# Optimization experiments

Hardware: AMD Instinct MI355X
Metric: run time of the kernel (lower is better)

The kernel has to match this reference:

```python
import jax, jax.numpy as jnp
import numpy as np

N, T, D, H = 32, 2048, 256, 256


def setup_inputs() -> dict:
    key = jax.random.key(0)
    k0, k1, k2, k3, k4 = jax.random.split(key, 5)
    std = 1.0 / np.sqrt(H + D)  # matches PTLSTM.reset()
    return {
        "x": jax.random.normal(k0, (N, T, D), dtype=jnp.float32),
        "state": jnp.zeros((N, 2 * H), dtype=jnp.float32),  # [h0 | c0]
        "w_ih": (jax.random.normal(k1, (4 * H, D)) * std).astype(jnp.float32),
        "w_hh": (jax.random.normal(k2, (4 * H, H)) * std).astype(jnp.float32),
        "b_ih": (jax.random.normal(k3, (4 * H,)) * std).astype(jnp.float32),
        "b_hh": (jax.random.normal(k4, (4 * H,)) * std).astype(jnp.float32),
    }


def reference(x, state, w_ih, w_hh, b_ih, b_hh):
    # Single-layer batch_first LSTM, PyTorch gate order (i, f, g, o).
    Hd = w_hh.shape[1]
    h0, c0 = state[:, :Hd], state[:, Hd:]
    # Precompute input-to-hidden projection for all timesteps (one big GEMM).
    xg = jnp.einsum('ntd,gd->ntg', x, w_ih) + (b_ih + b_hh)  # [N, T, 4H]

    def step(carry, xg_t):
        h, c = carry
        gates = xg_t + h @ w_hh.T  # [N, 4H]
        i, f, g, o = jnp.split(gates, 4, axis=-1)
        i = jax.nn.sigmoid(i)
        f = jax.nn.sigmoid(f)
        g = jnp.tanh(g)
        o = jax.nn.sigmoid(o)
        c = f * c + i * g
        h = o * jnp.tanh(c)
        return (h, c), h

    (hT, cT), out_t = jax.lax.scan(step, (h0, c0), jnp.swapaxes(xg, 0, 1))
    output = jnp.swapaxes(out_t, 0, 1)  # [N, T, H]
    outstate = jnp.concatenate([hT, cT], axis=1)  # [N, 2H]
    return output, outstate
```

## Files before the change

kernel.cpp:

```cpp
#include <hip/hip_runtime.h>

typedef _Float16 half2_t __attribute__((ext_vector_type(2)));
typedef __bf16   bf16x8  __attribute__((ext_vector_type(8)));
typedef float    f32x4   __attribute__((ext_vector_type(4)));
typedef unsigned short u16x8 __attribute__((ext_vector_type(8)));
typedef unsigned int  uint32;
typedef unsigned long long uint64;

#define LSTM_N 32
#define LSTM_T 2048
#define LSTM_D 256
#define LSTM_H 256
#define NG 1024
#define CH 256
#define NCH (LSTM_T / CH)
#define MCH (LSTM_N * CH)

#define OFF_XG   ((size_t)0)
#define SZ_XG    ((size_t)MCH * NG * 4)
#define OFF_WIHB (OFF_XG + SZ_XG)
#define SZ_WIHB  ((size_t)NG * LSTM_D * 2)
#define OFF_BIAS (OFF_WIHB + SZ_WIHB)
#define SZ_BIAS  ((size_t)4096)
#define OFF_WPK  (OFF_BIAS + SZ_BIAS)
#define SZ_WPK   ((size_t)2 * 32 * 512 * 16)
#define OFF_CST  (OFF_WPK + SZ_WPK)
#define SZ_CST   ((size_t)LSTM_N * 256 * 4)
#define OFF_HST  (OFF_CST + SZ_CST)
#define SZ_HST   ((size_t)LSTM_N * 128 * 4)
#define OFF_HX   (OFF_HST + SZ_HST)
#define SZ_HX    ((size_t)LSTM_N * 2 * 2 * 64 * 8)

#if defined(__has_builtin)
#if __has_builtin(__builtin_amdgcn_fdot2)
#define HAVE_FDOT2 1
#endif
#endif

__device__ __forceinline__ float fdot2(uint32 w, uint32 h, float acc) {
#ifdef HAVE_FDOT2
  return __builtin_amdgcn_fdot2(__builtin_bit_cast(half2_t, w),
                                __builtin_bit_cast(half2_t, h), acc, false);
#else
  half2_t wv = __builtin_bit_cast(half2_t, w);
  half2_t hv = __builtin_bit_cast(half2_t, h);
  float r = fmaf((float)wv.x, (float)hv.x, acc);
  return fmaf((float)wv.y, (float)hv.y, r);
#endif
}

__device__ __forceinline__ float sigm(float x) { return 1.f / (1.f + __expf(-x)); }
__device__ __forceinline__ float tanh_fast(float x) { return 2.f / (1.f + __expf(-2.f * x)) - 1.f; }

__device__ __forceinline__ unsigned short f2bf(float f) {
  uint32 u = __builtin_bit_cast(uint32, f);
  uint32 r = (u + 0x7FFFu + ((u >> 16) & 1u)) >> 16;
  return (unsigned short)r;
}

__device__ __forceinline__ float bfly8(const float a[8], int kap) {
  float k0[4], g0[4];
  const bool b4 = (kap & 4) != 0;
#pragma unroll
  for (int v = 0; v < 4; ++v) {
    k0[v] = b4 ? a[v + 4] : a[v];
    g0[v] = b4 ? a[v] : a[v + 4];
  }
#pragma unroll
  for (int v = 0; v < 4; ++v) k0[v] += __shfl_xor(g0[v], 4, 64);
  float k1[2], g1[2];
  const bool b2 = (kap & 2) != 0;
#pragma unroll
  for (int v = 0; v < 2; ++v) {
    k1[v] = b2 ? k0[v + 2] : k0[v];
    g1[v] = b2 ? k0[v] : k0[v + 2];
  }
#pragma unroll
  for (int v = 0; v < 2; ++v) k1[v] += __shfl_xor(g1[v], 2, 64);
  const bool b1 = (kap & 1) != 0;
  float k2 = b1 ? k1[1] : k1[0];
  float g2 = b1 ? k1[0] : k1[1];
  return k2 + __shfl_xor(g2, 1, 64);
}


__global__ void cvt_bf16_k(const float* __restrict__ src, unsigned short* __restrict__ dst, int n) {
  int i = blockIdx.x * blockDim.x + threadIdx.x;
  if (4 * i + 3 < n) {
    float4 v = ((const float4*)src)[i];
    ushort4 o;
    o.x = f2bf(v.x); o.y = f2bf(v.y); o.z = f2bf(v.z); o.w = f2bf(v.w);
    ((ushort4*)dst)[i] = o;
  }
}

__global__ void bias_sum_k(const float* __restrict__ bih, const float* __restrict__ bhh,
                           float* __restrict__ bias) {
  int g = blockIdx.x * blockDim.x + threadIdx.x;
  if (g < NG) bias[g] = bih[g] + bhh[g];
}

__global__ void wpack_k(const float* __restrict__ whh, uint32* __restrict__ wpk) {
  int e = blockIdx.x * blockDim.x + threadIdx.x;
  int p = e >> 16;
  int rem = e & 0xFFFF;
  int i = rem >> 9;
  int t = rem & 511;
  int rho = i >> 4, j = i & 15;
  int kap = t & 7, rg = t >> 3;
  int lr = 8 * rg + rho;
  int q = lr >> 7, u = lr & 127;
  int r = q * 256 + 128 * p + u;
  int k = (j < 8) ? (128 * p + 16 * kap + 2 * j)
                  : (128 * (1 - p) + 16 * kap + 2 * (j - 8));
  half2_t h;
  h.x = (_Float16)whh[r * 256 + k];
  h.y = (_Float16)whh[r * 256 + k + 1];
  wpk[((p * 32 + (i >> 2)) * 512 + t) * 4 + (i & 3)] = __builtin_bit_cast(uint32, h);
}

__global__ void state_init_k(const float* __restrict__ state, float* __restrict__ cst,
                             uint32* __restrict__ hst, uint64* __restrict__ hx) {
  int i = blockIdx.x * blockDim.x + threadIdx.x;
  int n = i >> 8, j = i & 255;
  cst[i] = state[n * 512 + 256 + j];
  if ((j & 1) == 0) {
    half2_t h2;
    h2.x = (_Float16)state[n * 512 + j];
    h2.y = (_Float16)state[n * 512 + j + 1];
    hst[(n << 7) + (j >> 1)] = __builtin_bit_cast(uint32, h2);
  }
  hx[i] = 0ull;
}

__global__ __launch_bounds__(256) void gemm_xg(const float* __restrict__ x,
                                               const unsigned short* __restrict__ wb,
                                               const float* __restrict__ bias,
                                               float* __restrict__ xg, int ch) {
  __shared__ unsigned short As[128 * 40];
  __shared__ unsigned short Bs[128 * 40];
  const int tid = threadIdx.x;
  const int m0 = blockIdx.y * 128;
  const int g0 = blockIdx.x * 128;
  const int w = tid >> 6;
  const int lane = tid & 63;
  const int wm = (w >> 1) * 64, wn = (w & 1) * 64;
  const int row_l = tid >> 2;
  const int q = tid & 3;
  const int lr = lane & 15, kg = lane >> 4;

  size_t grow[2];
#pragma unroll
  for (int r = 0; r < 2; ++r) {
    int gm = m0 + row_l + 64 * r;
    grow[r] = (size_t)(gm >> 8) * LSTM_T + (size_t)ch * CH + (gm & 255);
  }

  f32x4 acc[4][4];
#pragma unroll
  for (int i = 0; i < 4; ++i)
#pragma unroll
    for (int j = 0; j < 4; ++j) acc[i][j] = (f32x4){0.f, 0.f, 0.f, 0.f};

  for (int kt = 0; kt < 8; ++kt) {
#pragma unroll
    for (int r = 0; r < 2; ++r) {
      int row = row_l + 64 * r;
      const float* ap = x + grow[r] * 256 + kt * 32 + q * 8;
      float4 v0 = *(const float4*)ap;
      float4 v1 = *(const float4*)(ap + 4);
      u16x8 o;
      o[0] = f2bf(v0.x); o[1] = f2bf(v0.y); o[2] = f2bf(v0.z); o[3] = f2bf(v0.w);
      o[4] = f2bf(v1.x); o[5] = f2bf(v1.y); o[6] = f2bf(v1.z); o[7] = f2bf(v1.w);
      *(uint4*)((char*)As + row * 80 + q * 16) = __builtin_bit_cast(uint4, o);
      uint4 bv = *(const uint4*)(wb + (size_t)(g0 + row) * 256 + kt * 32 + q * 8);
      *(uint4*)((char*)Bs + row * 80 + q * 16) = bv;
    }
    __syncthreads();
    bf16x8 af[4], bfr[4];
#pragma unroll
    for (int i = 0; i < 4; ++i)
      af[i] = __builtin_bit_cast(bf16x8, *(const uint4*)((char*)As + (wm + 16 * i + lr) * 80 + kg * 16));
#pragma unroll
    for (int j = 0; j < 4; ++j)
      bfr[j] = __builtin_bit_cast(bf16x8, *(const uint4*)((char*)Bs + (wn + 16 * j + lr) * 80 + kg * 16));
#pragma unroll
    for (int i = 0; i < 4; ++i)
#pragma unroll
      for (int j = 0; j < 4; ++j)
        acc[i][j] = __builtin_amdgcn_mfma_f32_16x16x32_bf16(af[i], bfr[j], acc[i][j], 0, 0, 0);
    __syncthreads();
  }
#pragma unroll
  for (int j = 0; j < 4; ++j) {
    int gc = g0 + wn + 16 * j + lr;
    float bj = bias[gc];
#pragma unroll
    for (int i = 0; i < 4; ++i) {
#pragma unroll
      for (int r = 0; r < 4; ++r) {
        int m = m0 + wm + 16 * i + kg * 4 + r;
        xg[(size_t)m * NG + gc] = acc[i][j][r] + bj;
      }
    }
  }
}

__global__ __launch_bounds__(512, 2) void lstm_scan(const float* __restrict__ xg,
                                                    const uint4* __restrict__ wpk4,
                                                    float* __restrict__ cst,
                                                    uint32* __restrict__ hst,
                                                    uint64* __restrict__ hx,
                                                    float* __restrict__ out, int ch) {
  __shared__ float actb[512];
  __shared__ uint32 hbuf[128];

  const int tid = threadIdx.x;
  const int b = blockIdx.x;
  const int n = b & 31;
  const int p = b >> 5;
  const int kap = tid & 7;
  const int rg = tid >> 3;
  const int lrf = 8 * rg + kap;
  const int q = lrf >> 7, u = lrf & 127;
  const int grow = q * 256 + 128 * p + u;

  uint32 wr[128];
#pragma unroll
  for (int ig = 0; ig < 32; ++ig) {
    uint4 v = wpk4[(p * 32 + ig) * 512 + tid];
    wr[4 * ig + 0] = v.x; wr[4 * ig + 1] = v.y; wr[4 * ig + 2] = v.z; wr[4 * ig + 3] = v.w;
  }
  float c = 0.f;
  if (tid < 128) {
    c = cst[n * 256 + 128 * p + tid];
    hbuf[tid] = hst[n * 128 + tid];
  }
  __syncthreads();

  const float* xgn = xg + (size_t)n * CH * NG;
  float* outb = out + ((size_t)n * LSTM_T + (size_t)ch * CH) * LSTM_H;
  uint64* hx_own  = hx + (size_t)((n * 2 + p) * 2) * 64;
  uint64* hx_peer = hx + (size_t)((n * 2 + (1 - p)) * 2) * 64;
  const int gsbase = ch * CH;
  const int ownbase  = 64 * p + 8 * kap;
  const int peerbase = 64 * (1 - p) + 8 * kap;

  float xpre = xgn[grow];

  for (int tt = 0; tt < CH; ++tt) {
    if (tt > 0 && tid < 64) {
      const uint32 gs = (uint32)(gsbase + tt);
      uint64 v;
      do {
        v = __hip_atomic_load(&hx_peer[(gs & 1) * 64 + tid], __ATOMIC_RELAXED,
                              __HIP_MEMORY_SCOPE_AGENT);
      } while ((uint32)(v >> 32) != gs);
      hbuf[64 * (1 - p) + tid] = (uint32)v;
    }
    uint32 hro[8];
    *(uint4*)&hro[0] = *(const uint4*)&hbuf[ownbase];
    *(uint4*)&hro[4] = *(const uint4*)&hbuf[ownbase + 4];
    float acc[8];
#pragma unroll
    for (int rho = 0; rho < 8; ++rho) {
      float a = 0.f;
#pragma unroll
      for (int j = 0; j < 8; ++j) a = fdot2(wr[rho * 16 + j], hro[j], a);
      acc[rho] = a;
    }
    __syncthreads();
    uint32 hrp[8];
    *(uint4*)&hrp[0] = *(const uint4*)&hbuf[peerbase];
    *(uint4*)&hrp[4] = *(const uint4*)&hbuf[peerbase + 4];
#pragma unroll
    for (int rho = 0; rho < 8; ++rho) {
      float a = acc[rho];
#pragma unroll
      for (int j = 0; j < 8; ++j) a = fdot2(wr[rho * 16 + 8 + j], hrp[j], a);
      acc[rho] = a;
    }
    float s = bfly8(acc, kap);
    float pre = s + xpre;
    if (tt < CH - 1) xpre = xgn[(size_t)(tt + 1) * NG + grow];
    float a0 = (q == 2) ? tanh_fast(pre) : sigm(pre);
    actb[lrf] = a0;
    __syncthreads();
    if (tid < 128) {
      float gi = actb[tid];
      float gf = actb[128 + tid];
      float gg = actb[256 + tid];
      float go = actb[384 + tid];
      c = gf * c + gi * gg;
      float h = go * tanh_fast(c);
      _Float16 hf = (_Float16)h;
      ((unsigned short*)hbuf)[128 * p + tid] = __builtin_bit_cast(unsigned short, hf);
      outb[(size_t)tt * LSTM_H + 128 * p + tid] = h;
      if (ch == NCH - 1 && tt == CH - 1) {
        float* os = out + (size_t)LSTM_N * LSTM_T * LSTM_H + n * 512;
        os[128 * p + tid] = h;
        os[256 + 128 * p + tid] = c;
      }
    }
    __syncthreads();
    if (tt < CH - 1 && tid < 64) {
      const uint32 gs = (uint32)(gsbase + tt + 1);
      uint64 v = (uint64)hbuf[64 * p + tid] | ((uint64)gs << 32);
      __hip_atomic_store(&hx_own[(gs & 1) * 64 + tid], v, __ATOMIC_RELAXED,
                         __HIP_MEMORY_SCOPE_AGENT);
    }
  }
  if (tid < 128) cst[n * 256 + 128 * p + tid] = c;
  if (tid < 64) hst[n * 128 + 64 * p + tid] = hbuf[64 * p + tid];
}

extern "C" void kernel_launch(void* const* d_in, const int* in_sizes, int n_in,
                              void* d_out, int out_size, void* d_ws, size_t ws_size,
                              hipStream_t stream) {
  const float* x   = (const float*)d_in[0];
  const float* st  = (const float*)d_in[1];
  const float* wih = (const float*)d_in[2];
  const float* whh = (const float*)d_in[3];
  const float* bih = (const float*)d_in[4];
  const float* bhh = (const float*)d_in[5];
  float* out = (float*)d_out;
  char* ws = (char*)d_ws;

  float* xg = (float*)(ws + OFF_XG);
  unsigned short* wihb = (unsigned short*)(ws + OFF_WIHB);
  float* bias = (float*)(ws + OFF_BIAS);
  uint32* wpk = (uint32*)(ws + OFF_WPK);
  float* cst = (float*)(ws + OFF_CST);
  uint32* hst = (uint32*)(ws + OFF_HST);
  uint64* hx = (uint64*)(ws + OFF_HX);

  cvt_bf16_k<<<(NG * LSTM_D / 4 + 255) / 256, 256, 0, stream>>>(wih, wihb, NG * LSTM_D);
  bias_sum_k<<<4, 256, 0, stream>>>(bih, bhh, bias);
  wpack_k<<<512, 256, 0, stream>>>(whh, wpk);
  state_init_k<<<32, 256, 0, stream>>>(st, cst, hst, hx);

  for (int ch = 0; ch < NCH; ++ch) {
    gemm_xg<<<dim3(NG / 128, MCH / 128), 256, 0, stream>>>(x, wihb, bias, xg, ch);
    lstm_scan<<<64, 512, 0, stream>>>(xg, (const uint4*)wpk, cst, hst, hx, out, ch);
  }
}
```

Before: 3.450 ms.

## Run recurrent matvec on MFMA with 16-sequence batches per block

The recurrent h@W_hh product now uses f16 MFMA instructions. Each block handles 16 batch sequences and one half of the hidden units, instead of one sequence per block using fdot2 and butterfly shuffles. The xg GEMM output is transposed to a gate-major layout so each lane can load its gate preactivations directly. Gate activations and the cell update are done in registers, which removes the shared-memory activation exchange and one barrier per step. Only 4 of the 16 launched blocks do work, so far fewer CUs run the serial scan, and the peer exchange per step now moves more data through atomics.

```diff
diff --git a/kernel.cpp b/kernel.cpp
--- a/kernel.cpp
+++ b/kernel.cpp
@@ -1,6 +1,7 @@
 #include <hip/hip_runtime.h>
 
 typedef _Float16 half2_t __attribute__((ext_vector_type(2)));
+typedef _Float16 f16x8   __attribute__((ext_vector_type(8)));
 typedef __bf16   bf16x8  __attribute__((ext_vector_type(8)));
 typedef float    f32x4   __attribute__((ext_vector_type(4)));
 typedef unsigned short u16x8 __attribute__((ext_vector_type(8)));
@@ -17,7 +18,7 @@
 #define MCH (LSTM_N * CH)
 
 #define OFF_XG   ((size_t)0)
-#define SZ_XG    ((size_t)MCH * NG * 4)
+#define SZ_XG    ((size_t)NG * MCH * 4)
 #define OFF_WIHB (OFF_XG + SZ_XG)
 #define SZ_WIHB  ((size_t)NG * LSTM_D * 2)
 #define OFF_BIAS (OFF_WIHB + SZ_WIHB)
@@ -29,25 +30,7 @@
 #define OFF_HST  (OFF_CST + SZ_CST)
 #define SZ_HST   ((size_t)LSTM_N * 128 * 4)
 #define OFF_HX   (OFF_HST + SZ_HST)
-#define SZ_HX    ((size_t)LSTM_N * 2 * 2 * 64 * 8)
-
-#if defined(__has_builtin)
-#if __has_builtin(__builtin_amdgcn_fdot2)
-#define HAVE_FDOT2 1
-#endif
-#endif
-
-__device__ __forceinline__ float fdot2(uint32 w, uint32 h, float acc) {
-#ifdef HAVE_FDOT2
-  return __builtin_amdgcn_fdot2(__builtin_bit_cast(half2_t, w),
-                                __builtin_bit_cast(half2_t, h), acc, false);
-#else
-  half2_t wv = __builtin_bit_cast(half2_t, w);
-  half2_t hv = __builtin_bit_cast(half2_t, h);
-  float r = fmaf((float)wv.x, (float)hv.x, acc);
-  return fmaf((float)wv.y, (float)hv.y, r);
-#endif
-}
+#define SZ_HX    ((size_t)2 * 2 * 2 * 1024 * 8)
 
 __device__ __forceinline__ float sigm(float x) { return 1.f / (1.f + __expf(-x)); }
 __device__ __forceinline__ float tanh_fast(float x) { return 2.f / (1.f + __expf(-2.f * x)) - 1.f; }
@@ -56,31 +39,6 @@
   uint32 u = __builtin_bit_cast(uint32, f);
   uint32 r = (u + 0x7FFFu + ((u >> 16) & 1u)) >> 16;
   return (unsigned short)r;
-}
-
-__device__ __forceinline__ float bfly8(const float a[8], int kap) {
-  float k0[4], g0[4];
-  const bool b4 = (kap & 4) != 0;
-#pragma unroll
-  for (int v = 0; v < 4; ++v) {
-    k0[v] = b4 ? a[v + 4] : a[v];
-    g0[v] = b4 ? a[v] : a[v + 4];
-  }
-#pragma unroll
-  for (int v = 0; v < 4; ++v) k0[v] += __shfl_xor(g0[v], 4, 64);
-  float k1[2], g1[2];
-  const bool b2 = (kap & 2) != 0;
-#pragma unroll
-  for (int v = 0; v < 2; ++v) {
-    k1[v] = b2 ? k0[v + 2] : k0[v];
-    g1[v] = b2 ? k0[v] : k0[v + 2];
-  }
-#pragma unroll
-  for (int v = 0; v < 2; ++v) k1[v] += __shfl_xor(g1[v], 2, 64);
-  const bool b1 = (kap & 1) != 0;
-  float k2 = b1 ? k1[1] : k1[0];
-  float g2 = b1 ? k1[0] : k1[1];
-  return k2 + __shfl_xor(g2, 1, 64);
 }
 
 
@@ -103,20 +61,17 @@
 __global__ void wpack_k(const float* __restrict__ whh, uint32* __restrict__ wpk) {
   int e = blockIdx.x * blockDim.x + threadIdx.x;
   int p = e >> 16;
-  int rem = e & 0xFFFF;
-  int i = rem >> 9;
-  int t = rem & 511;
-  int rho = i >> 4, j = i & 15;
-  int kap = t & 7, rg = t >> 3;
-  int lr = 8 * rg + rho;
-  int q = lr >> 7, u = lr & 127;
-  int r = q * 256 + 128 * p + u;
-  int k = (j < 8) ? (128 * p + 16 * kap + 2 * j)
-                  : (128 * (1 - p) + 16 * kap + 2 * (j - 8));
+  int i = (e >> 9) & 127;
+  int t = e & 511;
+  int q = i >> 5, kc = (i >> 2) & 7, rr = i & 3;
+  int w = t >> 6, l = t & 63;
+  int grow = q * 256 + 128 * p + 16 * w + (l & 15);
+  int kb = (kc < 4) ? (128 * p + 32 * kc) : (128 * (1 - p) + 32 * (kc - 4));
+  int k = kb + (l >> 4) * 8 + 2 * rr;
   half2_t h;
-  h.x = (_Float16)whh[r * 256 + k];
-  h.y = (_Float16)whh[r * 256 + k + 1];
-  wpk[((p * 32 + (i >> 2)) * 512 + t) * 4 + (i & 3)] = __builtin_bit_cast(uint32, h);
+  h.x = (_Float16)whh[grow * 256 + k];
+  h.y = (_Float16)whh[grow * 256 + k + 1];
+  wpk[((p * 32 + q * 8 + kc) * 512 + t) * 4 + rr] = __builtin_bit_cast(uint32, h);
 }
 
 __global__ void state_init_k(const float* __restrict__ state, float* __restrict__ cst,
@@ -133,28 +88,25 @@
   hx[i] = 0ull;
 }
 
-__global__ __launch_bounds__(256) void gemm_xg(const float* __restrict__ x,
-                                               const unsigned short* __restrict__ wb,
-                                               const float* __restrict__ bias,
-                                               float* __restrict__ xg, int ch) {
+__global__ __launch_bounds__(256) void gemm_xgp(const float* __restrict__ x,
+                                                const unsigned short* __restrict__ wb,
+                                                const float* __restrict__ bias,
+                                                float* __restrict__ xgp, int ch) {
   __shared__ unsigned short As[128 * 40];
   __shared__ unsigned short Bs[128 * 40];
   const int tid = threadIdx.x;
   const int m0 = blockIdx.y * 128;
-  const int g0 = blockIdx.x * 128;
+  const int c0 = blockIdx.x * 128;
   const int w = tid >> 6;
   const int lane = tid & 63;
   const int wm = (w >> 1) * 64, wn = (w & 1) * 64;
-  const int row_l = tid >> 2;
-  const int q = tid & 3;
   const int lr = lane & 15, kg = lane >> 4;
-
-  size_t grow[2];
-#pragma unroll
-  for (int r = 0; r < 2; ++r) {
-    int gm = m0 + row_l + 64 * r;
-    grow[r] = (size_t)(gm >> 8) * LSTM_T + (size_t)ch * CH + (gm & 255);
-  }
+  const int srow = tid >> 1, kh = tid & 1;
+
+  const int cbl = c0 + srow;
+  const float* xb = x + (size_t)(cbl & 31) * LSTM_T * LSTM_D
+                      + (size_t)(ch * CH + (cbl >> 5)) * LSTM_D + kh * 16;
+  const unsigned short* ab = wb + (size_t)(m0 + srow) * 256 + kh * 16;
 
   f32x4 acc[4][4];
 #pragma unroll
@@ -163,18 +115,23 @@
     for (int j = 0; j < 4; ++j) acc[i][j] = (f32x4){0.f, 0.f, 0.f, 0.f};
 
   for (int kt = 0; kt < 8; ++kt) {
-#pragma unroll
-    for (int r = 0; r < 2; ++r) {
-      int row = row_l + 64 * r;
-      const float* ap = x + grow[r] * 256 + kt * 32 + q * 8;
-      float4 v0 = *(const float4*)ap;
-      float4 v1 = *(const float4*)(ap + 4);
-      u16x8 o;
-      o[0] = f2bf(v0.x); o[1] = f2bf(v0.y); o[2] = f2bf(v0.z); o[3] = f2bf(v0.w);
-      o[4] = f2bf(v1.x); o[5] = f2bf(v1.y); o[6] = f2bf(v1.z); o[7] = f2bf(v1.w);
-      *(uint4*)((char*)As + row * 80 + q * 16) = __builtin_bit_cast(uint4, o);
-      uint4 bv = *(const uint4*)(wb + (size_t)(g0 + row) * 256 + kt * 32 + q * 8);
-      *(uint4*)((char*)Bs + row * 80 + q * 16) = bv;
+    {
+      uint4 a0 = *(const uint4*)(ab + kt * 32);
+      uint4 a1 = *(const uint4*)(ab + kt * 32 + 8);
+      *(uint4*)((char*)As + srow * 80 + kh * 32) = a0;
+      *(uint4*)((char*)As + srow * 80 + kh * 32 + 16) = a1;
+      const float* bp = xb + kt * 32;
+      float4 v0 = *(const float4*)(bp + 0);
+      float4 v1 = *(const float4*)(bp + 4);
+      float4 v2 = *(const float4*)(bp + 8);
+      float4 v3 = *(const float4*)(bp + 12);
+      u16x8 o0, o1;
+      o0[0] = f2bf(v0.x); o0[1] = f2bf(v0.y); o0[2] = f2bf(v0.z); o0[3] = f2bf(v0.w);
+      o0[4] = f2bf(v1.x); o0[5] = f2bf(v1.y); o0[6] = f2bf(v1.z); o0[7] = f2bf(v1.w);
+      o1[0] = f2bf(v2.x); o1[1] = f2bf(v2.y); o1[2] = f2bf(v2.z); o1[3] = f2bf(v2.w);
+      o1[4] = f2bf(v3.x); o1[5] = f2bf(v3.y); o1[6] = f2bf(v3.z); o1[7] = f2bf(v3.w);
+      *(uint4*)((char*)Bs + srow * 80 + kh * 32) = __builtin_bit_cast(uint4, o0);
+      *(uint4*)((char*)Bs + srow * 80 + kh * 32 + 16) = __builtin_bit_cast(uint4, o1);
     }
     __syncthreads();
     bf16x8 af[4], bfr[4];
@@ -191,127 +148,154 @@
         acc[i][j] = __builtin_amdgcn_mfma_f32_16x16x32_bf16(af[i], bfr[j], acc[i][j], 0, 0, 0);
     __syncthreads();
   }
-#pragma unroll
-  for (int j = 0; j < 4; ++j) {
-    int gc = g0 + wn + 16 * j + lr;
-    float bj = bias[gc];
-#pragma unroll
-    for (int i = 0; i < 4; ++i) {
-#pragma unroll
-      for (int r = 0; r < 4; ++r) {
-        int m = m0 + wm + 16 * i + kg * 4 + r;
-        xg[(size_t)m * NG + gc] = acc[i][j][r] + bj;
-      }
-    }
-  }
-}
-
-__global__ __launch_bounds__(512, 2) void lstm_scan(const float* __restrict__ xg,
+  float bias_v[4][4];
+#pragma unroll
+  for (int i = 0; i < 4; ++i)
+#pragma unroll
+    for (int r = 0; r < 4; ++r) bias_v[i][r] = bias[m0 + wm + 16 * i + kg * 4 + r];
+#pragma unroll
+  for (int i = 0; i < 4; ++i)
+#pragma unroll
+    for (int j = 0; j < 4; ++j)
+#pragma unroll
+      for (int r = 0; r < 4; ++r)
+        xgp[(size_t)(m0 + wm + 16 * i + kg * 4 + r) * MCH + (c0 + wn + 16 * j + lr)]
+            = acc[i][j][r] + bias_v[i][r];
+}
+
+__global__ __launch_bounds__(512, 2) void lstm_scan(const float* __restrict__ xgp,
                                                     const uint4* __restrict__ wpk4,
                                                     float* __restrict__ cst,
                                                     uint32* __restrict__ hst,
                                                     uint64* __restrict__ hx,
                                                     float* __restrict__ out, int ch) {
-  __shared__ float actb[512];
-  __shared__ uint32 hbuf[128];
-
-  const int tid = threadIdx.x;
+  __shared__ uint32 hbuf[16][132];
   const int b = blockIdx.x;
-  const int n = b & 31;
-  const int p = b >> 5;
-  const int kap = tid & 7;
-  const int rg = tid >> 3;
-  const int lrf = 8 * rg + kap;
-  const int q = lrf >> 7, u = lrf & 127;
-  const int grow = q * 256 + 128 * p + u;
-
-  uint32 wr[128];
-#pragma unroll
-  for (int ig = 0; ig < 32; ++ig) {
-    uint4 v = wpk4[(p * 32 + ig) * 512 + tid];
-    wr[4 * ig + 0] = v.x; wr[4 * ig + 1] = v.y; wr[4 * ig + 2] = v.z; wr[4 * ig + 3] = v.w;
-  }
-  float c = 0.f;
-  if (tid < 128) {
-    c = cst[n * 256 + 128 * p + tid];
-    hbuf[tid] = hst[n * 128 + tid];
-  }
+  if ((b & 7) >= 2) return;
+  const int g = b & 1;
+  const int p = b >> 3;
+  const int t = threadIdx.x;
+  const int w = t >> 6, l = t & 63;
+  const int ls = l & 15, lq = l >> 4;
+
+  uint4 wfr[32];
+#pragma unroll
+  for (int i = 0; i < 32; ++i) wfr[i] = wpk4[(p * 32 + i) * 512 + t];
+
+  {
+    int s = t >> 5, m4 = (t & 31) * 4;
+    *(uint4*)&hbuf[s][m4] = *(const uint4*)&hst[(16 * g + s) * 128 + m4];
+  }
+  const int ubase = 16 * w + 4 * lq;
+  const int n = 16 * g + ls;
+  float4 cc4 = *(const float4*)&cst[n * 256 + 128 * p + ubase];
+  float cc[4] = {cc4.x, cc4.y, cc4.z, cc4.w};
   __syncthreads();
 
-  const float* xgn = xg + (size_t)n * CH * NG;
-  float* outb = out + ((size_t)n * LSTM_T + (size_t)ch * CH) * LSTM_H;
-  uint64* hx_own  = hx + (size_t)((n * 2 + p) * 2) * 64;
-  uint64* hx_peer = hx + (size_t)((n * 2 + (1 - p)) * 2) * 64;
   const int gsbase = ch * CH;
-  const int ownbase  = 64 * p + 8 * kap;
-  const int peerbase = 64 * (1 - p) + 8 * kap;
-
-  float xpre = xgn[grow];
+  uint64* hx_own  = hx + (size_t)(g * 2 + p) * 2048;
+  uint64* hx_peer = hx + (size_t)(g * 2 + (1 - p)) * 2048;
+
+  const int rowb = 128 * p + ubase;
+  const float* xgl = xgp + (size_t)rowb * MCH + n;
+  float* outb = out + ((size_t)n * LSTM_T + (size_t)ch * CH) * 256 + 128 * p + ubase;
+
+  const int own_u32 = 64 * p;
+  const int peer_u32 = 64 * (1 - p);
+  const int slotb = ls * 64 + 8 * w + 2 * lq;
+
+  float xpre[16];
+#pragma unroll
+  for (int q = 0; q < 4; ++q)
+#pragma unroll
+    for (int r = 0; r < 4; ++r)
+      xpre[q * 4 + r] = xgl[(size_t)(q * 256 + r) * MCH];
 
   for (int tt = 0; tt < CH; ++tt) {
-    if (tt > 0 && tid < 64) {
+    f32x4 acc[4];
+#pragma unroll
+    for (int q = 0; q < 4; ++q) acc[q] = (f32x4){0.f, 0.f, 0.f, 0.f};
+    uint4 bb[4];
+#pragma unroll
+    for (int kc = 0; kc < 4; ++kc)
+      bb[kc] = *(const uint4*)&hbuf[ls][own_u32 + 16 * kc + 4 * lq];
+#pragma unroll
+    for (int kc = 0; kc < 4; ++kc) {
+      f16x8 bv = __builtin_bit_cast(f16x8, bb[kc]);
+#pragma unroll
+      for (int q = 0; q < 4; ++q)
+        acc[q] = __builtin_amdgcn_mfma_f32_16x16x32_f16(
+            __builtin_bit_cast(f16x8, wfr[q * 8 + kc]), bv, acc[q], 0, 0, 0);
+    }
+    if (tt > 0) {
       const uint32 gs = (uint32)(gsbase + tt);
-      uint64 v;
+      uint64* sp = &hx_peer[(size_t)(gs & 1) * 1024 + 2 * t];
+      uint64 v0, v1;
       do {
-        v = __hip_atomic_load(&hx_peer[(gs & 1) * 64 + tid], __ATOMIC_RELAXED,
-                              __HIP_MEMORY_SCOPE_AGENT);
-      } while ((uint32)(v >> 32) != gs);
-      hbuf[64 * (1 - p) + tid] = (uint32)v;
-    }
-    uint32 hro[8];
-    *(uint4*)&hro[0] = *(const uint4*)&hbuf[ownbase];
-    *(uint4*)&hro[4] = *(const uint4*)&hbuf[ownbase + 4];
-    float acc[8];
-#pragma unroll
-    for (int rho = 0; rho < 8; ++rho) {
-      float a = 0.f;
-#pragma unroll
-      for (int j = 0; j < 8; ++j) a = fdot2(wr[rho * 16 + j], hro[j], a);
-      acc[rho] = a;
+        v0 = __hip_atomic_load(sp, __ATOMIC_RELAXED, __HIP_MEMORY_SCOPE_AGENT);
+      } while ((uint32)(v0 >> 32) != gs);
+      do {
+        v1 = __hip_atomic_load(sp + 1, __ATOMIC_RELAXED, __HIP_MEMORY_SCOPE_AGENT);
+      } while ((uint32)(v1 >> 32) != gs);
+      uint2 pv; pv.x = (uint32)v0; pv.y = (uint32)v1;
+      *(uint2*)&hbuf[t >> 5][peer_u32 + 2 * (t & 31)] = pv;
     }
     __syncthreads();
-    uint32 hrp[8];
-    *(uint4*)&hrp[0] = *(const uint4*)&hbuf[peerbase];
-    *(uint4*)&hrp[4] = *(const uint4*)&hbuf[peerbase + 4];
-#pragma unroll
-    for (int rho = 0; rho < 8; ++rho) {
-      float a = acc[rho];
-#pragma unroll
-      for (int j = 0; j < 8; ++j) a = fdot2(wr[rho * 16 + 8 + j], hrp[j], a);
-      acc[rho] = a;
-    }
-    float s = bfly8(acc, kap);
-    float pre = s + xpre;
-    if (tt < CH - 1) xpre = xgn[(size_t)(tt + 1) * NG + grow];
-    float a0 = (q == 2) ? tanh_fast(pre) : sigm(pre);
-    actb[lrf] = a0;
+#pragma unroll
+    for (int kc = 0; kc < 4; ++kc)
+      bb[kc] = *(const uint4*)&hbuf[ls][peer_u32 + 16 * kc + 4 * lq];
+#pragma unroll
+    for (int kc = 0; kc < 4; ++kc) {
+      f16x8 bv = __builtin_bit_cast(f16x8, bb[kc]);
+#pragma unroll
+      for (int q = 0; q < 4; ++q)
+        acc[q] = __builtin_amdgcn_mfma_f32_16x16x32_f16(
+            __builtin_bit_cast(f16x8, wfr[q * 8 + 4 + kc]), bv, acc[q], 0, 0, 0);
+    }
+    float hv[4];
+#pragma unroll
+    for (int r = 0; r < 4; ++r) {
+      float gi = sigm(acc[0][r] + xpre[0 + r]);
+      float gf = sigm(acc[1][r] + xpre[4 + r]);
+      float gg = tanh_fast(acc[2][r] + xpre[8 + r]);
+      float go = sigm(acc[3][r] + xpre[12 + r]);
+      float c2 = gf * cc[r] + gi * gg;
+      cc[r] = c2;
+      hv[r] = go * tanh_fast(c2);
+    }
+    half2_t h01, h23;
+    h01.x = (_Float16)hv[0]; h01.y = (_Float16)hv[1];
+    h23.x = (_Float16)hv[2]; h23.y = (_Float16)hv[3];
+    uint32 hu0 = __builtin_bit_cast(uint32, h01);
+    uint32 hu1 = __builtin_bit_cast(uint32, h23);
+    if (tt < CH - 1) {
+      const uint32 gs2 = (uint32)(gsbase + tt + 1);
+      uint64* dp = &hx_own[(size_t)(gs2 & 1) * 1024 + slotb];
+      __hip_atomic_store(dp, (uint64)hu0 | ((uint64)gs2 << 32),
+                         __ATOMIC_RELAXED, __HIP_MEMORY_SCOPE_AGENT);
+      __hip_atomic_store(dp + 1, (uint64)hu1 | ((uint64)gs2 << 32),
+                         __ATOMIC_RELAXED, __HIP_MEMORY_SCOPE_AGENT);
+    }
+    uint2 hw; hw.x = hu0; hw.y = hu1;
+    *(uint2*)&hbuf[ls][own_u32 + 8 * w + 2 * lq] = hw;
+    *(float4*)&outb[(size_t)tt * 256] = make_float4(hv[0], hv[1], hv[2], hv[3]);
+    if (ch == NCH - 1 && tt == CH - 1) {
+      float* os = out + (size_t)LSTM_N * LSTM_T * LSTM_H + n * 512 + 128 * p + ubase;
+      *(float4*)os = make_float4(hv[0], hv[1], hv[2], hv[3]);
+      *(float4*)(os + 256) = make_float4(cc[0], cc[1], cc[2], cc[3]);
+    }
+    if (tt < CH - 1) {
+#pragma unroll
+      for (int q = 0; q < 4; ++q)
+#pragma unroll
+        for (int r = 0; r < 4; ++r)
+          xpre[q * 4 + r] = xgl[(size_t)(q * 256 + r) * MCH + (size_t)(tt + 1) * 32];
+    }
     __syncthreads();
-    if (tid < 128) {
-      float gi = actb[tid];
-      float gf = actb[128 + tid];
-      float gg = actb[256 + tid];
-      float go = actb[384 + tid];
-      c = gf * c + gi * gg;
-      float h = go * tanh_fast(c);
-      _Float16 hf = (_Float16)h;
-      ((unsigned short*)hbuf)[128 * p + tid] = __builtin_bit_cast(unsigned short, hf);
-      outb[(size_t)tt * LSTM_H + 128 * p + tid] = h;
-      if (ch == NCH - 1 && tt == CH - 1) {
-        float* os = out + (size_t)LSTM_N * LSTM_T * LSTM_H + n * 512;
-        os[128 * p + tid] = h;
-        os[256 + 128 * p + tid] = c;
-      }
-    }
-    __syncthreads();
-    if (tt < CH - 1 && tid < 64) {
-      const uint32 gs = (uint32)(gsbase + tt + 1);
-      uint64 v = (uint64)hbuf[64 * p + tid] | ((uint64)gs << 32);
-      __hip_atomic_store(&hx_own[(gs & 1) * 64 + tid], v, __ATOMIC_RELAXED,
-                         __HIP_MEMORY_SCOPE_AGENT);
-    }
-  }
-  if (tid < 128) cst[n * 256 + 128 * p + tid] = c;
-  if (tid < 64) hst[n * 128 + 64 * p + tid] = hbuf[64 * p + tid];
+  }
+  *(float4*)&cst[n * 256 + 128 * p + ubase] = make_float4(cc[0], cc[1], cc[2], cc[3]);
+  uint2 hfin = *(uint2*)&hbuf[ls][own_u32 + 8 * w + 2 * lq];
+  *(uint2*)&hst[n * 128 + 64 * p + 8 * w + 2 * lq] = hfin;
 }
 
 extern "C" void kernel_launch(void* const* d_in, const int* in_sizes, int n_in,
@@ -326,7 +310,7 @@
   float* out = (float*)d_out;
   char* ws = (char*)d_ws;
 
-  float* xg = (float*)(ws + OFF_XG);
+  float* xgp = (float*)(ws + OFF_XG);
   unsigned short* wihb = (unsigned short*)(ws + OFF_WIHB);
   float* bias = (float*)(ws + OFF_BIAS);
   uint32* wpk = (uint32*)(ws + OFF_WPK);
@@ -340,7 +324,7 @@
   state_init_k<<<32, 256, 0, stream>>>(st, cst, hst, hx);
 
   for (int ch = 0; ch < NCH; ++ch) {
-    gemm_xg<<<dim3(NG / 128, MCH / 128), 256, 0, stream>>>(x, wihb, bias, xg, ch);
-    lstm_scan<<<64, 512, 0, stream>>>(xg, (const uint4*)wpk, cst, hst, hx, out, ch);
-  }
-}
+    gemm_xgp<<<dim3(MCH / 128, NG / 128), 256, 0, stream>>>(x, wihb, bias, xgp, ch);
+    lstm_scan<<<16, 512, 0, stream>>>(xgp, (const uint4*)wpk, cst, hst, hx, out, ch);
+  }
+}
```

Result: slower. 5.882 ms (+70.5%).

## Have every thread poll peer hidden state directly and double-buffer own h

Applied to the files above, without the earlier changes.

Each thread now loads its eight peer h words straight from the global exchange buffer with atomics and spins on the step tags itself. The own-half dot products run while those loads are in flight. One LDS barrier per step is removed, and the own hidden state moves to a double-buffered shared array. Producer threads pack two fp16 values through a shuffle and publish right after computing h, not after the barrier. The change trades more global polling traffic, since all 512 threads poll instead of 64, for a shorter critical path between the two cooperating blocks. The row mapping also changes, and launch bounds drop to one block per SM.

```diff
diff --git a/kernel.cpp b/kernel.cpp
--- a/kernel.cpp
+++ b/kernel.cpp
@@ -206,112 +206,126 @@
   }
 }
 
-__global__ __launch_bounds__(512, 2) void lstm_scan(const float* __restrict__ xg,
+__global__ __launch_bounds__(512, 1) void lstm_scan(const float* __restrict__ xg,
                                                     const uint4* __restrict__ wpk4,
                                                     float* __restrict__ cst,
                                                     uint32* __restrict__ hst,
                                                     uint64* __restrict__ hx,
                                                     float* __restrict__ out, int ch) {
   __shared__ float actb[512];
-  __shared__ uint32 hbuf[128];
-
-  const int tid = threadIdx.x;
+  __shared__ uint32 hown[2][64];
+
   const int b = blockIdx.x;
   const int n = b & 31;
   const int p = b >> 5;
-  const int kap = tid & 7;
-  const int rg = tid >> 3;
-  const int lrf = 8 * rg + kap;
-  const int q = lrf >> 7, u = lrf & 127;
-  const int grow = q * 256 + 128 * p + u;
+  const int t = threadIdx.x;
+  const int kap = t & 7;
+  const int q = t >> 7;
+  const int u = t & 127;
+  const int R = q * 256 + 128 * p + u;
 
   uint32 wr[128];
 #pragma unroll
   for (int ig = 0; ig < 32; ++ig) {
-    uint4 v = wpk4[(p * 32 + ig) * 512 + tid];
+    uint4 v = wpk4[(p * 32 + ig) * 512 + t];
     wr[4 * ig + 0] = v.x; wr[4 * ig + 1] = v.y; wr[4 * ig + 2] = v.z; wr[4 * ig + 3] = v.w;
   }
   float c = 0.f;
-  if (tid < 128) {
-    c = cst[n * 256 + 128 * p + tid];
-    hbuf[tid] = hst[n * 128 + tid];
-  }
+  if (t < 128) c = cst[n * 256 + 128 * p + t];
+  if (t < 64) hown[0][t] = hst[n * 128 + 64 * p + t];
   __syncthreads();
 
   const float* xgn = xg + (size_t)n * CH * NG;
   float* outb = out + ((size_t)n * LSTM_T + (size_t)ch * CH) * LSTM_H;
-  uint64* hx_own  = hx + (size_t)((n * 2 + p) * 2) * 64;
-  uint64* hx_peer = hx + (size_t)((n * 2 + (1 - p)) * 2) * 64;
+  uint64* hx_own  = hx + (size_t)(n * 2 + p) * 128;
+  uint64* hx_peer = hx + (size_t)(n * 2 + (1 - p)) * 128;
   const int gsbase = ch * CH;
-  const int ownbase  = 64 * p + 8 * kap;
-  const int peerbase = 64 * (1 - p) + 8 * kap;
-
-  float xpre = xgn[grow];
+
+  float xcur = xgn[R];
 
   for (int tt = 0; tt < CH; ++tt) {
-    if (tt > 0 && tid < 64) {
-      const uint32 gs = (uint32)(gsbase + tt);
-      uint64 v;
+    const uint32 gs = (uint32)(gsbase + tt);
+    uint64 pv[8];
+    uint32 hrp[8];
+    if (tt == 0) {
+#pragma unroll
+      for (int m = 0; m < 8; ++m) hrp[m] = hst[n * 128 + 64 * (1 - p) + 8 * kap + m];
+    } else {
+      uint64* sp = &hx_peer[(size_t)(gs & 1) * 64 + 8 * kap];
+#pragma unroll
+      for (int ss = 0; ss < 8; ++ss)
+        pv[ss] = __hip_atomic_load(&sp[ss], __ATOMIC_RELAXED, __HIP_MEMORY_SCOPE_AGENT);
+    }
+    float xnext = (tt < CH - 1) ? xgn[(size_t)(tt + 1) * NG + R] : 0.f;
+    uint32 hro[8];
+    *(uint4*)&hro[0] = *(const uint4*)&hown[tt & 1][8 * kap];
+    *(uint4*)&hro[4] = *(const uint4*)&hown[tt & 1][8 * kap + 4];
+    float acc[8];
+#pragma unroll
+    for (int j = 0; j < 8; ++j) {
+      float a = 0.f;
+#pragma unroll
+      for (int m = 0; m < 8; ++m) a = fdot2(wr[j * 16 + m], hro[m], a);
+      acc[j] = a;
+    }
+    if (tt > 0) {
+      bool ok;
       do {
-        v = __hip_atomic_load(&hx_peer[(gs & 1) * 64 + tid], __ATOMIC_RELAXED,
-                              __HIP_MEMORY_SCOPE_AGENT);
-      } while ((uint32)(v >> 32) != gs);
-      hbuf[64 * (1 - p) + tid] = (uint32)v;
-    }
-    uint32 hro[8];
-    *(uint4*)&hro[0] = *(const uint4*)&hbuf[ownbase];
-    *(uint4*)&hro[4] = *(const uint4*)&hbuf[ownbase + 4];
-    float acc[8];
-#pragma unroll
-    for (int rho = 0; rho < 8; ++rho) {
-      float a = 0.f;
-#pragma unroll
-      for (int j = 0; j < 8; ++j) a = fdot2(wr[rho * 16 + j], hro[j], a);
-      acc[rho] = a;
-    }
+        ok = true;
+#pragma unroll
+        for (int ss = 0; ss < 8; ++ss) ok &= ((uint32)(pv[ss] >> 32) == gs);
+        if (!ok) {
+          uint64* sp = &hx_peer[(size_t)(gs & 1) * 64 + 8 * kap];
+#pragma unroll
+          for (int ss = 0; ss < 8; ++ss)
+            pv[ss] = __hip_atomic_load(&sp[ss], __ATOMIC_RELAXED, __HIP_MEMORY_SCOPE_AGENT);
+        }
+      } while (!ok);
+#pragma unroll
+      for (int ss = 0; ss < 8; ++ss) hrp[ss] = (uint32)pv[ss];
+    }
+#pragma unroll
+    for (int j = 0; j < 8; ++j) {
+      float a = acc[j];
+#pragma unroll
+      for (int m = 0; m < 8; ++m) a = fdot2(wr[j * 16 + 8 + m], hrp[m], a);
+      acc[j] = a;
+    }
+    float s = bfly8(acc, kap);
+    float pre = s + xcur;
+    xcur = xnext;
+    float a0 = (q == 2) ? tanh_fast(pre) : sigm(pre);
+    actb[t] = a0;
     __syncthreads();
-    uint32 hrp[8];
-    *(uint4*)&hrp[0] = *(const uint4*)&hbuf[peerbase];
-    *(uint4*)&hrp[4] = *(const uint4*)&hbuf[peerbase + 4];
-#pragma unroll
-    for (int rho = 0; rho < 8; ++rho) {
-      float a = acc[rho];
-#pragma unroll
-      for (int j = 0; j < 8; ++j) a = fdot2(wr[rho * 16 + 8 + j], hrp[j], a);
-      acc[rho] = a;
-    }
-    float s = bfly8(acc, kap);
-    float pre = s + xpre;
-    if (tt < CH - 1) xpre = xgn[(size_t)(tt + 1) * NG + grow];
-    float a0 = (q == 2) ? tanh_fast(pre) : sigm(pre);
-    actb[lrf] = a0;
-    __syncthreads();
-    if (tid < 128) {
-      float gi = actb[tid];
-      float gf = actb[128 + tid];
-      float gg = actb[256 + tid];
-      float go = actb[384 + tid];
+    if (t < 128) {
+      float gi = actb[t];
+      float gf = actb[128 + t];
+      float gg = actb[256 + t];
+      float go = actb[384 + t];
       c = gf * c + gi * gg;
       float h = go * tanh_fast(c);
       _Float16 hf = (_Float16)h;
-      ((unsigned short*)hbuf)[128 * p + tid] = __builtin_bit_cast(unsigned short, hf);
-      outb[(size_t)tt * LSTM_H + 128 * p + tid] = h;
+      unsigned short hu = __builtin_bit_cast(unsigned short, hf);
+      ((unsigned short*)&hown[(tt + 1) & 1][0])[t] = hu;
+      outb[(size_t)tt * LSTM_H + 128 * p + t] = h;
+      uint32 hz = (uint32)hu;
+      uint32 hn = (uint32)__shfl_xor((int)hz, 1, 64);
+      if (tt < CH - 1 && (t & 1) == 0) {
+        const uint32 gs2 = gs + 1;
+        uint64 msg = (uint64)(hz | (hn << 16)) | ((uint64)gs2 << 32);
+        __hip_atomic_store(&hx_own[(size_t)(gs2 & 1) * 64 + (t >> 1)], msg,
+                           __ATOMIC_RELAXED, __HIP_MEMORY_SCOPE_AGENT);
+      }
       if (ch == NCH - 1 && tt == CH - 1) {
         float* os = out + (size_t)LSTM_N * LSTM_T * LSTM_H + n * 512;
-        os[128 * p + tid] = h;
-        os[256 + 128 * p + tid] = c;
+        os[128 * p + t] = h;
+        os[256 + 128 * p + t] = c;
       }
     }
     __syncthreads();
-    if (tt < CH - 1 && tid < 64) {
-      const uint32 gs = (uint32)(gsbase + tt + 1);
-      uint64 v = (uint64)hbuf[64 * p + tid] | ((uint64)gs << 32);
-      __hip_atomic_store(&hx_own[(gs & 1) * 64 + tid], v, __ATOMIC_RELAXED,
-                         __HIP_MEMORY_SCOPE_AGENT);
-    }
-  }
-  if (tid < 128) cst[n * 256 + 128 * p + tid] = c;
-  if (tid < 64) hst[n * 128 + 64 * p + tid] = hbuf[64 * p + tid];
+  }
+  if (t < 128) cst[n * 256 + 128 * p + t] = c;
+  if (t < 64) hst[n * 128 + 64 * p + t] = hown[0][t];
 }
 
 extern "C" void kernel_launch(void* const* d_in, const int* in_sizes, int n_in,
```

New measurement: 4.888 ms. 41.7% more time.
